# Performance work log

Hardware: AMD Instinct MI355X
Metric: run time of the kernel (lower is better)

The kernel has to match this reference:

```python
import jax, jax.numpy as jnp
import numpy as np

EMBED_DIM = 1024


def setup_inputs() -> dict:
    key = jax.random.key(0)
    ks = jax.random.split(key, 9)
    d = EMBED_DIM
    s = 1.0 / np.sqrt(d)
    x = jax.random.normal(ks[0], (4, 4096, d), dtype=jnp.float32)
    Wq = jax.random.normal(ks[1], (d, d), dtype=jnp.float32) * s
    bq = jax.random.normal(ks[2], (d,), dtype=jnp.float32) * 0.01
    Wk = jax.random.normal(ks[3], (d, d), dtype=jnp.float32) * s
    bk = jax.random.normal(ks[4], (d,), dtype=jnp.float32) * 0.01
    Wv = jax.random.normal(ks[5], (d, d), dtype=jnp.float32) * s
    bv = jax.random.normal(ks[6], (d,), dtype=jnp.float32) * 0.01
    Wo = jax.random.normal(ks[7], (d, d), dtype=jnp.float32) * s
    bo = jax.random.normal(ks[8], (d,), dtype=jnp.float32) * 0.01
    return {"x": x, "Wq": Wq, "bq": bq, "Wk": Wk, "bk": bk,
            "Wv": Wv, "bv": bv, "Wo": Wo, "bo": bo}


def reference(x, Wq, bq, Wk, bk, Wv, bv, Wo, bo):
    # x: [b, s, d]; single-head attention, scale = 1/sqrt(d)
    b, s, d = x.shape
    q = x @ Wq + bq
    k = x @ Wk + bk
    v = x @ Wv + bv
    scale = 1.0 / jnp.sqrt(jnp.asarray(d, x.dtype))
    scores = jnp.einsum('bqd,bkd->bqk', q, k) * scale  # [b, s, s]
    causal = jnp.tril(jnp.ones((s, s), dtype=bool))
    scores = jnp.where(causal, scores, jnp.asarray(-jnp.inf, scores.dtype))
    attn = jax.nn.softmax(scores, axis=-1)
    ctx = jnp.einsum('bqk,bkd->bqd', attn, v)
    return ctx @ Wo + bo
```

## Files before the change

kernel.cpp:

```cpp
#include <hip/hip_runtime.h>


typedef unsigned short u16;
typedef __attribute__((ext_vector_type(4))) unsigned short u16x4;
typedef __attribute__((ext_vector_type(8))) unsigned short u16x8;
typedef __attribute__((ext_vector_type(8))) __bf16 bf16x8;
typedef __attribute__((ext_vector_type(4))) float f32x4;

typedef const __attribute__((address_space(1))) void* as1cp;
typedef __attribute__((address_space(3))) void* as3p;

struct GemmPtrs {
  const u16* A[4];
  const u16* B[4];
  const float* bias[4];
  void* C[4];
};
struct TransPtrs {
  const void* in[4];
  u16* out[4];
};
struct SmPtrs {
  u16* P[4];
};

__device__ __forceinline__ u16 f2bf(float f) {
  union { float f; unsigned int i; } c; c.f = f;
  unsigned int r = c.i + 0x7fffu + ((c.i >> 16) & 1u);
  return (u16)(r >> 16);
}
__device__ __forceinline__ float bf2f(u16 u) {
  union { unsigned int i; float f; } c; c.i = ((unsigned int)u) << 16;
  return c.f;
}

__global__ __launch_bounds__(256) void cast_f32_bf16(const float* __restrict__ in,
                                                     u16* __restrict__ out, int n4) {
  int i = blockIdx.x * blockDim.x + threadIdx.x;
  if (i >= n4) return;
  float4 v = ((const float4*)in)[i];
  u16x4 u;
  u.x = f2bf(v.x); u.y = f2bf(v.y); u.z = f2bf(v.z); u.w = f2bf(v.w);
  ((u16x4*)out)[i] = u;
}

template <bool IN_F32>
__global__ __launch_bounds__(256) void transpose_to_bf16(TransPtrs tp, int R, int C) {
  __shared__ u16 t[32][34];
  int z = blockIdx.z;
  int tx = threadIdx.x, ty = threadIdx.y;
  int c0 = blockIdx.x * 32, r0 = blockIdx.y * 32;
#pragma unroll
  for (int dy = 0; dy < 4; ++dy) {
    int r = r0 + ty + dy * 8;
    int c = c0 + tx;
    u16 hv;
    if (IN_F32) hv = f2bf(((const float*)tp.in[z])[(size_t)r * C + c]);
    else        hv = ((const u16*)tp.in[z])[(size_t)r * C + c];
    t[ty + dy * 8][tx] = hv;
  }
  __syncthreads();
  u16* op = tp.out[z];
#pragma unroll
  for (int dy = 0; dy < 4; ++dy) {
    int a = ty + dy * 8;
    op[(size_t)(c0 + a) * R + r0 + tx] = t[tx][a];
  }
}

__global__ __launch_bounds__(256) void softmax_causal(SmPtrs sp) {
  int row = blockIdx.x;
  u16* P = sp.P[blockIdx.y];
  int tid = threadIdx.x;
  int lane = tid & 63, wv = tid >> 6;
  u16x8* prow = (u16x8*)(P + (size_t)row * 4096);
  int nch = (row >> 3) + 1;
  int fend = ((row >> 7) + 1) << 4;
  int c0 = tid, c1 = tid + 256;
  bool a0 = c0 < nch, a1 = c1 < nch;
  float vals[16];
  float lmax = -3.0e38f;
  if (a0) {
    u16x8 u = prow[c0];
#pragma unroll
    for (int e = 0; e < 8; ++e) {
      float f = (c0 * 8 + e <= row) ? bf2f(u[e]) : -3.0e38f;
      vals[e] = f; lmax = fmaxf(lmax, f);
    }
  } else {
#pragma unroll
    for (int e = 0; e < 8; ++e) vals[e] = -3.0e38f;
  }
  if (a1) {
    u16x8 u = prow[c1];
#pragma unroll
    for (int e = 0; e < 8; ++e) {
      float f = (c1 * 8 + e <= row) ? bf2f(u[e]) : -3.0e38f;
      vals[8 + e] = f; lmax = fmaxf(lmax, f);
    }
  } else {
#pragma unroll
    for (int e = 0; e < 8; ++e) vals[8 + e] = -3.0e38f;
  }
  __shared__ float red[8];
#pragma unroll
  for (int off = 32; off > 0; off >>= 1) lmax = fmaxf(lmax, __shfl_down(lmax, off, 64));
  if (lane == 0) red[wv] = lmax;
  __syncthreads();
  float m2 = fmaxf(fmaxf(red[0], red[1]), fmaxf(red[2], red[3]));
  float lsum = 0.f;
#pragma unroll
  for (int e = 0; e < 16; ++e) {
    float ev = __expf(vals[e] - m2);
    vals[e] = ev;
    lsum += ev;
  }
#pragma unroll
  for (int off = 32; off > 0; off >>= 1) lsum += __shfl_down(lsum, off, 64);
  if (lane == 0) red[4 + wv] = lsum;
  __syncthreads();
  float inv = 1.0f / (red[4] + red[5] + red[6] + red[7]);
  if (a0) {
    u16x8 u;
#pragma unroll
    for (int e = 0; e < 8; ++e) u[e] = f2bf(vals[e] * inv);
    prow[c0] = u;
  }
  if (a1) {
    u16x8 u;
#pragma unroll
    for (int e = 0; e < 8; ++e) u[e] = f2bf(vals[8 + e] * inv);
    prow[c1] = u;
  }
  u16x8 zz = (u16x8)(u16)0;
  for (int c = nch + tid; c < fend; c += 256) prow[c] = zz;
}

template <int MODE, bool OUT_BF16, bool HAS_BIAS, int MAXSLOT, int KDIM, int LDB>
__global__ __launch_bounds__(256) void gemm_persist(GemmPtrs p, int N, float cscale) {
  __shared__ __align__(16) u16 As[2][128 * 64];
  __shared__ __align__(16) u16 Bs[2][128 * 64];
  int b = blockIdx.x;
  int x = b & 7, q = b >> 3;
  int tid = threadIdx.x, lane = tid & 63, wv = tid >> 6;
  int wm = (wv >> 1) * 64, wn = (wv & 1) * 64;
  int lrow = lane & 15, lquad = lane >> 4;
  int srow = lane >> 3, scol = ((lane & 7) ^ srow) * 8;

  struct TP { const u16* A; const u16* B; int niter, tm, tn, z; };
  auto tileOf = [&](int s) {
    TP t;
    if (MODE == 0) {
      int c = x + 8 * (s * 8 + (q >> 3));
      t.z = c >> 7;
      t.tm = (c & 127) << 7; t.tn = (q & 7) << 7; t.niter = KDIM >> 6;
    } else if (MODE == 1) {
      int c = x + 8 * (s * 8 + (q >> 3));
      int tt = c * 8 + (q & 7);
      t.z = tt / 528; int L = tt - t.z * 528;
      int i = (int)((__fsqrt_rn(8.f * (float)L + 1.f) - 1.f) * 0.5f);
      while ((i + 1) * (i + 2) / 2 <= L) ++i;
      while (i * (i + 1) / 2 > L) --i;
      t.tm = i << 7; t.tn = (L - ((i * (i + 1)) >> 1)) << 7; t.niter = KDIM >> 6;
    } else if (MODE == 2) {
      int w = q & 15, h = w >> 3;
      int i = (s == 0) ? (h ? 15 - x : x) : (h ? 16 + x : 31 - x);
      t.z = q >> 4; t.tm = i << 7; t.tn = (w & 7) << 7; t.niter = (i + 1) * 2;
    } else {
      int c = x + 8 * (s * 8 + (q >> 3));
      t.z = 0; t.tm = c << 7; t.tn = (q & 7) << 7; t.niter = KDIM >> 6;
    }
    t.A = p.A[t.z] + (size_t)t.tm * KDIM;
    t.B = p.B[t.z] + (size_t)t.tn * LDB;
    return t;
  };
  int nslot = (MODE == 1) ? ((q >> 3) == 0 ? 5 : 4) : MAXSLOT;
  int total = (MODE == 2) ? 66 : nslot * (KDIM >> 6);

  int aoff = (wv * 32 + srow) * KDIM + scol;
  int boff = (wv * 32 + srow) * LDB + scol;

  TP st = tileOf(0);
  int stk = 0, sslot = 0;
  const u16* gA = st.A + aoff;
  const u16* gB = st.B + boff;

  auto stageTo = [&](int sb) {
#pragma unroll
    for (int tt = 0; tt < 4; ++tt) {
      __builtin_amdgcn_global_load_lds((as1cp)(gA + tt * 8 * KDIM),
                                       (as3p)&As[sb][(wv * 4 + tt) * 512], 16, 0, 0);
      __builtin_amdgcn_global_load_lds((as1cp)(gB + tt * 8 * LDB),
                                       (as3p)&Bs[sb][(wv * 4 + tt) * 512], 16, 0, 0);
    }
  };
  auto adv = [&]() {
    gA += 64; gB += 64;
    if (++stk == st.niter) {
      stk = 0;
      if (++sslot < nslot) {
        st = tileOf(sslot);
        gA = st.A + aoff;
        gB = st.B + boff;
      }
    }
  };

  f32x4 acc[4][4];
#pragma unroll
  for (int i = 0; i < 4; ++i)
#pragma unroll
    for (int j = 0; j < 4; ++j) acc[i][j] = (f32x4){0.f, 0.f, 0.f, 0.f};

  auto compute = [&](int cb) __attribute__((always_inline)) {
#pragma unroll
    for (int ks = 0; ks < 64; ks += 32) {
      bf16x8 af[4], bg[4];
#pragma unroll
      for (int mt = 0; mt < 4; ++mt) {
        int r = wm + mt * 16 + lrow;
        int jb = (ks >> 3) + lquad;
        af[mt] = *(const bf16x8*)&As[cb][r * 64 + ((jb ^ (r & 7)) << 3)];
      }
#pragma unroll
      for (int nt = 0; nt < 4; ++nt) {
        int r = wn + nt * 16 + lrow;
        int jb = (ks >> 3) + lquad;
        bg[nt] = *(const bf16x8*)&Bs[cb][r * 64 + ((jb ^ (r & 7)) << 3)];
      }
#pragma unroll
      for (int mt = 0; mt < 4; ++mt)
#pragma unroll
        for (int nt = 0; nt < 4; ++nt)
          acc[mt][nt] = __builtin_amdgcn_mfma_f32_16x16x32_bf16(af[mt], bg[nt], acc[mt][nt], 0, 0, 0);
    }
  };

  TP ct = st;
  int cit = 0, cslot = 0;
  auto epi = [&]() {
    if (++cit == ct.niter) {
      const float* bias = HAS_BIAS ? p.bias[ct.z] : nullptr;
#pragma unroll
      for (int mt = 0; mt < 4; ++mt) {
#pragma unroll
        for (int reg = 0; reg < 4; ++reg) {
          int r = ct.tm + wm + mt * 16 + lquad * 4 + reg;
#pragma unroll
          for (int nt = 0; nt < 4; ++nt) {
            int cidx = ct.tn + wn + nt * 16 + lrow;
            float vvv = acc[mt][nt][reg] * cscale;
            if (HAS_BIAS) vvv += bias[cidx];
            if (OUT_BF16) ((u16*)p.C[ct.z])[(size_t)r * N + cidx] = f2bf(vvv);
            else          ((float*)p.C[ct.z])[(size_t)r * N + cidx] = vvv;
          }
        }
      }
#pragma unroll
      for (int i = 0; i < 4; ++i)
#pragma unroll
        for (int j = 0; j < 4; ++j) acc[i][j] = (f32x4){0.f, 0.f, 0.f, 0.f};
      cit = 0;
      if (++cslot < nslot) ct = tileOf(cslot);
    }
  };

  stageTo(0);
  adv();
  for (int it = 0; it < total; it += 2) {
    if (it + 1 < total) {
      stageTo(1);
      adv();
      asm volatile("s_waitcnt vmcnt(8)" ::: "memory");
    } else {
      asm volatile("s_waitcnt vmcnt(0)" ::: "memory");
    }
    asm volatile("s_barrier" ::: "memory");
    compute(0);
    asm volatile("s_barrier" ::: "memory");
    epi();
    if (it + 2 < total) {
      stageTo(0);
      adv();
      asm volatile("s_waitcnt vmcnt(8)" ::: "memory");
    } else {
      asm volatile("s_waitcnt vmcnt(0)" ::: "memory");
    }
    asm volatile("s_barrier" ::: "memory");
    compute(1);
    asm volatile("s_barrier" ::: "memory");
    epi();
  }
}

extern "C" void kernel_launch(void* const* d_in, const int* in_sizes, int n_in,
                              void* d_out, int out_size, void* d_ws, size_t ws_size,
                              hipStream_t stream) {
  const float* x  = (const float*)d_in[0];
  const float* Wq = (const float*)d_in[1];
  const float* bq = (const float*)d_in[2];
  const float* Wk = (const float*)d_in[3];
  const float* bk = (const float*)d_in[4];
  const float* Wv = (const float*)d_in[5];
  const float* bv = (const float*)d_in[6];
  const float* Wo = (const float*)d_in[7];
  const float* bo = (const float*)d_in[8];

  const int S = 4096, D = 1024;
  const size_t XE = (size_t)4 * S * D;
  const size_t BSE = (size_t)S * D;

  char* ws = (char*)d_ws;
  u16* xb  = (u16*)(ws + 0);
  u16* q   = (u16*)(ws + 33554432);
  u16* k   = (u16*)(ws + 67108864);
  u16* v   = (u16*)(ws + 100663296);
  u16* ctx = (u16*)(ws + 134217728);
  u16* wqT = (u16*)(ws + 167772160);
  u16* wkT = wqT + 1048576;
  u16* wvT = wkT + 1048576;
  u16* woT = wvT + 1048576;
  u16* attn2 = (u16*)(ws + 176160768);
  u16* attn0 = (u16*)d_out;
  u16* attn1 = attn0 + (size_t)S * S;
  u16* attn3 = v;
  u16* vT = xb;
  u16* attn[4] = {attn0, attn1, attn2, attn3};

  cast_f32_bf16<<<(int)(XE / 4 / 256), 256, 0, stream>>>(x, xb, (int)(XE / 4));
  {
    TransPtrs tp = {{Wq, Wk, Wv, Wo}, {wqT, wkT, wvT, woT}};
    transpose_to_bf16<true><<<dim3(32, 32, 4), dim3(32, 8), 0, stream>>>(tp, D, D);
  }
  {
    GemmPtrs gp = {{xb, xb, xb, xb}, {wqT, wkT, wvT, wqT},
                   {bq, bk, bv, bq}, {q, k, v, q}};
    gemm_persist<0, true, true, 6, 1024, 1024><<<512, 256, 0, stream>>>(gp, D, 1.0f);
  }
  {
    TransPtrs tp = {{v, v + BSE, v + 2 * BSE, v + 3 * BSE},
                    {vT, vT + BSE, vT + 2 * BSE, vT + 3 * BSE}};
    transpose_to_bf16<false><<<dim3(D / 32, S / 32, 4), dim3(32, 8), 0, stream>>>(tp, S, D);
  }
  {
    GemmPtrs gp = {{q, q + BSE, q + 2 * BSE, q + 3 * BSE},
                   {k, k + BSE, k + 2 * BSE, k + 3 * BSE},
                   {nullptr, nullptr, nullptr, nullptr},
                   {attn[0], attn[1], attn[2], attn[3]}};
    gemm_persist<1, true, false, 5, 1024, 1024><<<512, 256, 0, stream>>>(gp, S, 0.03125f);
  }
  {
    SmPtrs sp = {{attn[0], attn[1], attn[2], attn[3]}};
    softmax_causal<<<dim3(S, 4), 256, 0, stream>>>(sp);
  }
  {
    GemmPtrs gp = {{attn[0], attn[1], attn[2], attn[3]},
                   {vT, vT + BSE, vT + 2 * BSE, vT + 3 * BSE},
                   {nullptr, nullptr, nullptr, nullptr},
                   {ctx, ctx + BSE, ctx + 2 * BSE, ctx + 3 * BSE}};
    gemm_persist<2, true, false, 2, 4096, 4096><<<512, 256, 0, stream>>>(gp, D, 1.0f);
  }
  {
    GemmPtrs gp = {{ctx, ctx, ctx, ctx}, {woT, woT, woT, woT},
                   {bo, bo, bo, bo}, {d_out, d_out, d_out, d_out}};
    gemm_persist<3, false, true, 2, 1024, 1024><<<512, 256, 0, stream>>>(gp, D, 1.0f);
  }
}
```

Before: 520.0 us.

## Add 256x256-tile persistent GEMM with 4-stage LDS pipeline for K=1024 GEMMs

Introduces a new persistent GEMM kernel that uses 256x256 output tiles, 512-thread blocks, a 4-slot direct-to-LDS pipeline and MFMA priority hints. It replaces the 128x128 kernel for the QKV projection, the causal QK^T scores (upper-triangle tile mapping) and the output projection. Larger tiles raise arithmetic intensity and cut global traffic. The cost is heavier register and LDS pressure and coarser load balance, with fewer tiles per GEMM.

```diff
diff --git a/kernel.cpp b/kernel.cpp
--- a/kernel.cpp
+++ b/kernel.cpp
@@ -134,6 +134,150 @@
   }
   u16x8 zz = (u16x8)(u16)0;
   for (int c = nch + tid; c < fend; c += 256) prow[c] = zz;
+}
+
+template <int MODE, bool OUT_BF16, bool HAS_BIAS>
+__global__ __launch_bounds__(512, 2) void gemm256(GemmPtrs p, int N, float cscale) {
+  __shared__ __align__(16) u16 As[4][8192];
+  __shared__ __align__(16) u16 Bs[4][8192];
+  const int b = blockIdx.x;
+  const int tid = threadIdx.x, lane = tid & 63, wv = tid >> 6;
+  const int wm = (wv >> 2) << 7, wn = (wv & 3) << 6;
+  const int lrow = lane & 15, lquad = lane >> 4;
+  const int xs = (lquad ^ ((lrow >> 1) & 3)) << 3;
+  const int aoff0 = (wm + lrow) * 32 + xs;
+  const int boff0 = (wn + lrow) * 32 + xs;
+  const int soff = (tid >> 2) * 1024 + (((tid & 3) ^ ((tid >> 3) & 3)) << 3);
+  const int nslot = (MODE == 1) ? (b < 32 ? 3 : 2) : (MODE == 0 ? 3 : 1);
+
+  struct TP { const u16* A; const u16* B; int tm, tn, z; };
+  auto tileOf = [&](int s) {
+    TP t;
+    if (MODE == 0) {
+      int g = s * 256 + b;
+      t.z = g >> 8; int i = g & 255;
+      t.tm = (i >> 2) << 8; t.tn = (i & 3) << 8;
+    } else if (MODE == 1) {
+      int g = s * 256 + b;
+      t.z = g / 136; int L = g - t.z * 136;
+      int i = (int)((__fsqrt_rn(8.f * (float)L + 1.f) - 1.f) * 0.5f);
+      while ((i + 1) * (i + 2) / 2 <= L) ++i;
+      while (i * (i + 1) / 2 > L) --i;
+      t.tm = i << 8; t.tn = (L - ((i * (i + 1)) >> 1)) << 8;
+    } else {
+      t.z = 0; t.tm = (b >> 2) << 8; t.tn = (b & 3) << 8;
+    }
+    t.A = p.A[t.z] + (size_t)t.tm * 1024;
+    t.B = p.B[t.z] + (size_t)t.tn * 1024;
+    return t;
+  };
+
+  auto stageA = [&](int slot, const u16* src) __attribute__((always_inline)) {
+    __builtin_amdgcn_global_load_lds((as1cp)src, (as3p)&As[slot][wv * 512], 16, 0, 0);
+    __builtin_amdgcn_global_load_lds((as1cp)(src + 131072),
+                                     (as3p)&As[slot][4096 + wv * 512], 16, 0, 0);
+  };
+  auto stageB = [&](int slot, const u16* src) __attribute__((always_inline)) {
+    __builtin_amdgcn_global_load_lds((as1cp)src, (as3p)&Bs[slot][wv * 512], 16, 0, 0);
+    __builtin_amdgcn_global_load_lds((as1cp)(src + 131072),
+                                     (as3p)&Bs[slot][4096 + wv * 512], 16, 0, 0);
+  };
+
+  f32x4 acc[8][4];
+
+  auto doBlock = [&](int tu, bool stg, const u16* sA, const u16* sB, int vm)
+      __attribute__((always_inline)) {
+    const int sT = (tu + 2) & 3;
+    bf16x8 af[4], bg[4];
+#pragma unroll
+    for (int m = 0; m < 4; ++m) af[m] = *(const bf16x8*)&As[tu][aoff0 + m * 512];
+#pragma unroll
+    for (int n = 0; n < 4; ++n) bg[n] = *(const bf16x8*)&Bs[tu][boff0 + n * 512];
+    if (stg) stageA(sT, sA);
+    asm volatile("s_barrier" ::: "memory");
+    __builtin_amdgcn_s_setprio(1);
+#pragma unroll
+    for (int m = 0; m < 4; ++m)
+#pragma unroll
+      for (int n = 0; n < 4; ++n)
+        acc[m][n] = __builtin_amdgcn_mfma_f32_16x16x32_bf16(af[m], bg[n], acc[m][n], 0, 0, 0);
+    __builtin_amdgcn_s_setprio(0);
+    asm volatile("s_barrier" ::: "memory");
+#pragma unroll
+    for (int m = 0; m < 4; ++m) af[m] = *(const bf16x8*)&As[tu][aoff0 + 2048 + m * 512];
+    if (stg) stageB(sT, sB);
+    asm volatile("s_barrier" ::: "memory");
+    __builtin_amdgcn_s_setprio(1);
+#pragma unroll
+    for (int m = 0; m < 4; ++m)
+#pragma unroll
+      for (int n = 0; n < 4; ++n)
+        acc[4 + m][n] = __builtin_amdgcn_mfma_f32_16x16x32_bf16(af[m], bg[n], acc[4 + m][n], 0, 0, 0);
+    __builtin_amdgcn_s_setprio(0);
+    if (vm == 4)      asm volatile("s_waitcnt vmcnt(4)" ::: "memory");
+    else if (vm == 0) asm volatile("s_waitcnt vmcnt(0)" ::: "memory");
+    asm volatile("s_barrier" ::: "memory");
+  };
+
+  TP ct = tileOf(0);
+  const u16* gA = ct.A + soff;
+  const u16* gB = ct.B + soff;
+  stageA(0, gA); stageB(0, gB);
+  stageA(1, gA + 32); stageB(1, gB + 32);
+  asm volatile("s_waitcnt vmcnt(4)" ::: "memory");
+  asm volatile("s_barrier" ::: "memory");
+
+  for (int s = 0;;) {
+#pragma unroll
+    for (int i = 0; i < 8; ++i)
+#pragma unroll
+      for (int j = 0; j < 4; ++j) acc[i][j] = (f32x4){0.f, 0.f, 0.f, 0.f};
+
+    for (int u = 0; u < 7; ++u) {
+#pragma unroll
+      for (int tu = 0; tu < 4; ++tu)
+        doBlock(tu, true, gA + (tu + 2) * 32, gB + (tu + 2) * 32, 4);
+      gA += 128; gB += 128;
+    }
+    doBlock(0, true, gA + 64, gB + 64, 4);
+    doBlock(1, true, gA + 96, gB + 96, 4);
+    doBlock(2, false, nullptr, nullptr, 0);
+    doBlock(3, false, nullptr, nullptr, -1);
+
+    bool more = (++s < nslot);
+    TP nt2;
+    if (more) {
+      nt2 = tileOf(s);
+      gA = nt2.A + soff; gB = nt2.B + soff;
+      stageA(0, gA); stageB(0, gB);
+    }
+    {
+      float bvv[4] = {0.f, 0.f, 0.f, 0.f};
+      if (HAS_BIAS) {
+        const float* bias = p.bias[ct.z];
+#pragma unroll
+        for (int n = 0; n < 4; ++n) bvv[n] = bias[ct.tn + wn + n * 16 + lrow];
+      }
+#pragma unroll
+      for (int m = 0; m < 8; ++m)
+#pragma unroll
+        for (int r = 0; r < 4; ++r) {
+          size_t row = (size_t)(ct.tm + wm + m * 16 + lquad * 4 + r);
+#pragma unroll
+          for (int n = 0; n < 4; ++n) {
+            int col = ct.tn + wn + n * 16 + lrow;
+            float vvv = acc[m][n][r] * cscale + bvv[n];
+            if (OUT_BF16) ((u16*)p.C[ct.z])[row * N + col] = f2bf(vvv);
+            else          ((float*)p.C[ct.z])[row * N + col] = vvv;
+          }
+        }
+    }
+    if (!more) return;
+    stageA(1, gA + 32); stageB(1, gB + 32);
+    asm volatile("s_waitcnt vmcnt(4)" ::: "memory");
+    asm volatile("s_barrier" ::: "memory");
+    ct = nt2;
+  }
 }
 
 template <int MODE, bool OUT_BF16, bool HAS_BIAS, int MAXSLOT, int KDIM, int LDB>
@@ -335,7 +479,7 @@
   {
     GemmPtrs gp = {{xb, xb, xb, xb}, {wqT, wkT, wvT, wqT},
                    {bq, bk, bv, bq}, {q, k, v, q}};
-    gemm_persist<0, true, true, 6, 1024, 1024><<<512, 256, 0, stream>>>(gp, D, 1.0f);
+    gemm256<0, true, true><<<256, 512, 0, stream>>>(gp, D, 1.0f);
   }
   {
     TransPtrs tp = {{v, v + BSE, v + 2 * BSE, v + 3 * BSE},
@@ -347,7 +491,7 @@
                    {k, k + BSE, k + 2 * BSE, k + 3 * BSE},
                    {nullptr, nullptr, nullptr, nullptr},
                    {attn[0], attn[1], attn[2], attn[3]}};
-    gemm_persist<1, true, false, 5, 1024, 1024><<<512, 256, 0, stream>>>(gp, S, 0.03125f);
+    gemm256<1, true, false><<<256, 512, 0, stream>>>(gp, S, 0.03125f);
   }
   {
     SmPtrs sp = {{attn[0], attn[1], attn[2], attn[3]}};
@@ -363,6 +507,6 @@
   {
     GemmPtrs gp = {{ctx, ctx, ctx, ctx}, {woT, woT, woT, woT},
                    {bo, bo, bo, bo}, {d_out, d_out, d_out, d_out}};
-    gemm_persist<3, false, true, 2, 1024, 1024><<<512, 256, 0, stream>>>(gp, D, 1.0f);
-  }
-}
+    gemm256<3, false, true><<<256, 512, 0, stream>>>(gp, D, 1.0f);
+  }
+}
```

Result: no change. 523.6 us (+0.7%).

## Replace persistent GEMM with 256x256-tile 512-thread kernel and dedicated PV kernel

Applied to the files above, without the earlier changes.

Replaces the 128x128, 256-thread persistent GEMM with a 256x256-tile, 8-wave kernel. It uses a 4-stage LDS ring with a K-step of 32, interleaved MFMA and LDS fragment loads, and s_setprio around the MFMA bursts. The causal P·V GEMM gets its own 128x256-tile kernel that pairs row blocks j and 31-j to balance the triangular work. The larger tiles raise arithmetic intensity and cut global traffic, and the deeper pipeline hides load latency. In exchange, register and LDS pressure go up, occupancy and the tile scheduling change, and the tile indexing is more intricate.

```diff
diff --git a/kernel.cpp b/kernel.cpp
--- a/kernel.cpp
+++ b/kernel.cpp
@@ -9,6 +9,8 @@
 
 typedef const __attribute__((address_space(1))) void* as1cp;
 typedef __attribute__((address_space(3))) void* as3p;
+
+template <int N> struct IC { static constexpr int v = N; };
 
 struct GemmPtrs {
   const u16* A[4];
@@ -136,161 +138,284 @@
   for (int c = nch + tid; c < fend; c += 256) prow[c] = zz;
 }
 
-template <int MODE, bool OUT_BF16, bool HAS_BIAS, int MAXSLOT, int KDIM, int LDB>
-__global__ __launch_bounds__(256) void gemm_persist(GemmPtrs p, int N, float cscale) {
-  __shared__ __align__(16) u16 As[2][128 * 64];
-  __shared__ __align__(16) u16 Bs[2][128 * 64];
-  int b = blockIdx.x;
-  int x = b & 7, q = b >> 3;
-  int tid = threadIdx.x, lane = tid & 63, wv = tid >> 6;
-  int wm = (wv >> 1) * 64, wn = (wv & 1) * 64;
-  int lrow = lane & 15, lquad = lane >> 4;
-  int srow = lane >> 3, scol = ((lane & 7) ^ srow) * 8;
-
-  struct TP { const u16* A; const u16* B; int niter, tm, tn, z; };
+template <int MODE, bool OUT_BF16, bool HAS_BIAS>
+__global__ __launch_bounds__(512, 2) void gemm256p(GemmPtrs p, int N, float cscale) {
+  __shared__ __align__(16) u16 As[4][8192];
+  __shared__ __align__(16) u16 Bs[4][8192];
+  const int b = blockIdx.x;
+  const int tid = threadIdx.x, lane = tid & 63, wv = tid >> 6;
+  const int wm = (wv >> 2) << 7, wn = (wv & 3) << 6;
+  const int lrow = lane & 15, lquad = lane >> 4;
+  const int xs = (lquad ^ ((lrow >> 1) & 3)) << 3;
+  const int aoff0 = (wm + lrow) * 32 + xs;
+  const int boff0 = (wn + lrow) * 32 + xs;
+  const int soff = (tid >> 2) * 1024 + (((tid & 3) ^ ((tid >> 3) & 3)) << 3);
+  const int x = b & 7, u = b >> 3;
+  const int nslot = (MODE == 1) ? (u < 4 ? 3 : 2) : (MODE == 0 ? 3 : 1);
+
+  struct TP { const u16* A; const u16* B; int tm, tn, z; };
   auto tileOf = [&](int s) {
     TP t;
     if (MODE == 0) {
-      int c = x + 8 * (s * 8 + (q >> 3));
-      t.z = c >> 7;
-      t.tm = (c & 127) << 7; t.tn = (q & 7) << 7; t.niter = KDIM >> 6;
+      int i = x * 32 + u;
+      t.z = s; t.tm = (i >> 2) << 8; t.tn = (i & 3) << 8;
     } else if (MODE == 1) {
-      int c = x + 8 * (s * 8 + (q >> 3));
-      int tt = c * 8 + (q & 7);
-      t.z = tt / 528; int L = tt - t.z * 528;
+      int g = x * 68 + s * 32 + u;
+      t.z = g / 136; int L = g - t.z * 136;
       int i = (int)((__fsqrt_rn(8.f * (float)L + 1.f) - 1.f) * 0.5f);
       while ((i + 1) * (i + 2) / 2 <= L) ++i;
       while (i * (i + 1) / 2 > L) --i;
-      t.tm = i << 7; t.tn = (L - ((i * (i + 1)) >> 1)) << 7; t.niter = KDIM >> 6;
-    } else if (MODE == 2) {
-      int w = q & 15, h = w >> 3;
-      int i = (s == 0) ? (h ? 15 - x : x) : (h ? 16 + x : 31 - x);
-      t.z = q >> 4; t.tm = i << 7; t.tn = (w & 7) << 7; t.niter = (i + 1) * 2;
+      t.tm = i << 8; t.tn = (L - ((i * (i + 1)) >> 1)) << 8;
     } else {
-      int c = x + 8 * (s * 8 + (q >> 3));
-      t.z = 0; t.tm = c << 7; t.tn = (q & 7) << 7; t.niter = KDIM >> 6;
-    }
-    t.A = p.A[t.z] + (size_t)t.tm * KDIM;
-    t.B = p.B[t.z] + (size_t)t.tn * LDB;
+      int i = x * 32 + u;
+      t.z = 0; t.tm = (i >> 2) << 8; t.tn = (i & 3) << 8;
+    }
+    t.A = p.A[t.z] + (size_t)t.tm * 1024;
+    t.B = p.B[t.z] + (size_t)t.tn * 1024;
     return t;
   };
-  int nslot = (MODE == 1) ? ((q >> 3) == 0 ? 5 : 4) : MAXSLOT;
-  int total = (MODE == 2) ? 66 : nslot * (KDIM >> 6);
-
-  int aoff = (wv * 32 + srow) * KDIM + scol;
-  int boff = (wv * 32 + srow) * LDB + scol;
-
-  TP st = tileOf(0);
-  int stk = 0, sslot = 0;
-  const u16* gA = st.A + aoff;
-  const u16* gB = st.B + boff;
-
-  auto stageTo = [&](int sb) {
-#pragma unroll
-    for (int tt = 0; tt < 4; ++tt) {
-      __builtin_amdgcn_global_load_lds((as1cp)(gA + tt * 8 * KDIM),
-                                       (as3p)&As[sb][(wv * 4 + tt) * 512], 16, 0, 0);
-      __builtin_amdgcn_global_load_lds((as1cp)(gB + tt * 8 * LDB),
-                                       (as3p)&Bs[sb][(wv * 4 + tt) * 512], 16, 0, 0);
-    }
-  };
+
+  const u16* gA; const u16* gB; int stk = 0, sslot = 0;
+  {
+    TP t0 = tileOf(0);
+    gA = t0.A + soff; gB = t0.B + soff;
+  }
   auto adv = [&]() {
-    gA += 64; gB += 64;
-    if (++stk == st.niter) {
-      stk = 0;
-      if (++sslot < nslot) {
-        st = tileOf(sslot);
-        gA = st.A + aoff;
-        gB = st.B + boff;
+    gA += 32; gB += 32;
+    ++stk;
+    if (stk == 32 && sslot < nslot) {
+      stk = 0; ++sslot;
+      if (sslot < nslot) {
+        TP t = tileOf(sslot);
+        gA = t.A + soff; gB = t.B + soff;
       }
     }
   };
 
-  f32x4 acc[4][4];
-#pragma unroll
-  for (int i = 0; i < 4; ++i)
+  f32x4 acc[8][4];
+#pragma unroll
+  for (int i = 0; i < 8; ++i)
 #pragma unroll
     for (int j = 0; j < 4; ++j) acc[i][j] = (f32x4){0.f, 0.f, 0.f, 0.f};
 
-  auto compute = [&](int cb) __attribute__((always_inline)) {
-#pragma unroll
-    for (int ks = 0; ks < 64; ks += 32) {
-      bf16x8 af[4], bg[4];
-#pragma unroll
-      for (int mt = 0; mt < 4; ++mt) {
-        int r = wm + mt * 16 + lrow;
-        int jb = (ks >> 3) + lquad;
-        af[mt] = *(const bf16x8*)&As[cb][r * 64 + ((jb ^ (r & 7)) << 3)];
-      }
-#pragma unroll
-      for (int nt = 0; nt < 4; ++nt) {
-        int r = wn + nt * 16 + lrow;
-        int jb = (ks >> 3) + lquad;
-        bg[nt] = *(const bf16x8*)&Bs[cb][r * 64 + ((jb ^ (r & 7)) << 3)];
-      }
-#pragma unroll
-      for (int mt = 0; mt < 4; ++mt)
-#pragma unroll
-        for (int nt = 0; nt < 4; ++nt)
-          acc[mt][nt] = __builtin_amdgcn_mfma_f32_16x16x32_bf16(af[mt], bg[nt], acc[mt][nt], 0, 0, 0);
-    }
-  };
-
-  TP ct = st;
-  int cit = 0, cslot = 0;
-  auto epi = [&]() {
-    if (++cit == ct.niter) {
-      const float* bias = HAS_BIAS ? p.bias[ct.z] : nullptr;
-#pragma unroll
-      for (int mt = 0; mt < 4; ++mt) {
-#pragma unroll
-        for (int reg = 0; reg < 4; ++reg) {
-          int r = ct.tm + wm + mt * 16 + lquad * 4 + reg;
-#pragma unroll
-          for (int nt = 0; nt < 4; ++nt) {
-            int cidx = ct.tn + wn + nt * 16 + lrow;
-            float vvv = acc[mt][nt][reg] * cscale;
-            if (HAS_BIAS) vvv += bias[cidx];
-            if (OUT_BF16) ((u16*)p.C[ct.z])[(size_t)r * N + cidx] = f2bf(vvv);
-            else          ((float*)p.C[ct.z])[(size_t)r * N + cidx] = vvv;
-          }
+  bf16x8 alo[4], ahi[4], bg0[4], bg1[4];
+
+#pragma unroll
+  for (int pt = 0; pt < 3; ++pt) {
+    __builtin_amdgcn_global_load_lds((as1cp)gA, (as3p)(As[pt] + wv * 512), 16, 0, 0);
+    __builtin_amdgcn_global_load_lds((as1cp)(gA + 131072), (as3p)(As[pt] + 4096 + wv * 512), 16, 0, 0);
+    __builtin_amdgcn_global_load_lds((as1cp)gB, (as3p)(Bs[pt] + wv * 512), 16, 0, 0);
+    __builtin_amdgcn_global_load_lds((as1cp)(gB + 131072), (as3p)(Bs[pt] + 4096 + wv * 512), 16, 0, 0);
+    adv();
+  }
+  asm volatile("s_waitcnt vmcnt(8)" ::: "memory");
+  asm volatile("s_barrier" ::: "memory");
+#pragma unroll
+  for (int m = 0; m < 4; ++m) alo[m] = *(const bf16x8*)&As[0][aoff0 + m * 512];
+#pragma unroll
+  for (int n = 0; n < 4; ++n) bg0[n] = *(const bf16x8*)&Bs[0][boff0 + n * 512];
+
+  auto kt = [&](auto CC, auto SS, auto VV, auto& BU, auto& BL)
+      __attribute__((always_inline)) {
+    constexpr int c = decltype(CC)::v;
+    constexpr int stg = decltype(SS)::v;
+    constexpr int vm = decltype(VV)::v;
+    __builtin_amdgcn_s_setprio(1);
+#pragma unroll
+    for (int m = 0; m < 4; ++m)
+#pragma unroll
+      for (int n = 0; n < 4; ++n)
+        acc[m][n] = __builtin_amdgcn_mfma_f32_16x16x32_bf16(alo[m], BU[n], acc[m][n], 0, 0, 0);
+    __builtin_amdgcn_s_setprio(0);
+#pragma unroll
+    for (int m = 0; m < 4; ++m)
+      ahi[m] = *(const bf16x8*)&As[c][aoff0 + 2048 + m * 512];
+    if constexpr (stg) {
+      __builtin_amdgcn_global_load_lds((as1cp)gA, (as3p)(As[(c + 3) & 3] + wv * 512), 16, 0, 0);
+      __builtin_amdgcn_global_load_lds((as1cp)(gA + 131072), (as3p)(As[(c + 3) & 3] + 4096 + wv * 512), 16, 0, 0);
+    }
+    if constexpr (vm == 6) asm volatile("s_waitcnt vmcnt(6)" ::: "memory");
+    else if constexpr (vm == 4) asm volatile("s_waitcnt vmcnt(4)" ::: "memory");
+    else if constexpr (vm == 0) asm volatile("s_waitcnt vmcnt(0)" ::: "memory");
+    asm volatile("s_barrier" ::: "memory");
+    __builtin_amdgcn_s_setprio(1);
+#pragma unroll
+    for (int m = 0; m < 4; ++m)
+#pragma unroll
+      for (int n = 0; n < 4; ++n)
+        acc[4 + m][n] = __builtin_amdgcn_mfma_f32_16x16x32_bf16(ahi[m], BU[n], acc[4 + m][n], 0, 0, 0);
+    __builtin_amdgcn_s_setprio(0);
+#pragma unroll
+    for (int m = 0; m < 4; ++m)
+      alo[m] = *(const bf16x8*)&As[(c + 1) & 3][aoff0 + m * 512];
+#pragma unroll
+    for (int n = 0; n < 4; ++n)
+      BL[n] = *(const bf16x8*)&Bs[(c + 1) & 3][boff0 + n * 512];
+    if constexpr (stg) {
+      __builtin_amdgcn_global_load_lds((as1cp)gB, (as3p)(Bs[(c + 3) & 3] + wv * 512), 16, 0, 0);
+      __builtin_amdgcn_global_load_lds((as1cp)(gB + 131072), (as3p)(Bs[(c + 3) & 3] + 4096 + wv * 512), 16, 0, 0);
+      adv();
+    }
+    asm volatile("s_barrier" ::: "memory");
+  };
+
+  auto epi = [&](int cs2) {
+    TP t = tileOf(cs2);
+    float bvv[4] = {0.f, 0.f, 0.f, 0.f};
+    if constexpr (HAS_BIAS) {
+#pragma unroll
+      for (int n = 0; n < 4; ++n) bvv[n] = p.bias[t.z][t.tn + wn + n * 16 + lrow];
+    }
+#pragma unroll
+    for (int m = 0; m < 8; ++m)
+#pragma unroll
+      for (int r = 0; r < 4; ++r) {
+        size_t row = (size_t)(t.tm + wm + m * 16 + lquad * 4 + r);
+#pragma unroll
+        for (int n = 0; n < 4; ++n) {
+          int col = t.tn + wn + n * 16 + lrow;
+          float vvv = acc[m][n][r] * cscale + bvv[n];
+          if (OUT_BF16) ((u16*)p.C[t.z])[row * N + col] = f2bf(vvv);
+          else          ((float*)p.C[t.z])[row * N + col] = vvv;
         }
       }
 #pragma unroll
-      for (int i = 0; i < 4; ++i)
-#pragma unroll
-        for (int j = 0; j < 4; ++j) acc[i][j] = (f32x4){0.f, 0.f, 0.f, 0.f};
-      cit = 0;
-      if (++cslot < nslot) ct = tileOf(cslot);
-    }
-  };
-
-  stageTo(0);
-  adv();
-  for (int it = 0; it < total; it += 2) {
-    if (it + 1 < total) {
-      stageTo(1);
-      adv();
-      asm volatile("s_waitcnt vmcnt(8)" ::: "memory");
-    } else {
-      asm volatile("s_waitcnt vmcnt(0)" ::: "memory");
-    }
+    for (int m2 = 0; m2 < 8; ++m2)
+#pragma unroll
+      for (int n2 = 0; n2 < 4; ++n2) acc[m2][n2] = (f32x4){0.f, 0.f, 0.f, 0.f};
+  };
+
+  const int total = nslot * 32;
+  int cs = 0;
+  for (int G = 0; G + 4 < total; G += 4) {
+    kt(IC<0>{}, IC<1>{}, IC<6>{}, bg0, bg1);
+    kt(IC<1>{}, IC<1>{}, IC<6>{}, bg1, bg0);
+    kt(IC<2>{}, IC<1>{}, IC<6>{}, bg0, bg1);
+    kt(IC<3>{}, IC<1>{}, IC<6>{}, bg1, bg0);
+    if (((G + 4) & 31) == 0) { epi(cs); ++cs; }
+  }
+  kt(IC<0>{}, IC<1>{}, IC<6>{}, bg0, bg1);
+  kt(IC<1>{}, IC<0>{}, IC<4>{}, bg1, bg0);
+  kt(IC<2>{}, IC<0>{}, IC<0>{}, bg0, bg1);
+  kt(IC<3>{}, IC<0>{}, IC<-1>{}, bg1, bg0);
+  epi(nslot - 1);
+}
+
+__global__ __launch_bounds__(512, 2) void gemm_pv(GemmPtrs p) {
+  __shared__ __align__(16) u16 As[4][4096];
+  __shared__ __align__(16) u16 Bs[4][8192];
+  const int b = blockIdx.x;
+  const int tid = threadIdx.x, lane = tid & 63, wv = tid >> 6;
+  const int wm = (wv >> 2) << 6, wn = (wv & 3) << 6;
+  const int lrow = lane & 15, lquad = lane >> 4;
+  const int xs = (lquad ^ ((lrow >> 1) & 3)) << 3;
+  const int aoff0 = (wm + lrow) * 32 + xs;
+  const int boff0 = (wn + lrow) * 32 + xs;
+  const int soff = (tid >> 2) * 4096 + (((tid & 3) ^ ((tid >> 3) & 3)) << 3);
+  const int x = b & 7, u = b >> 3;
+  const int P = x * 32 + u;
+  const int z = P >> 6, j = (P >> 2) & 15, n4 = P & 3;
+  const int i1 = j, i2 = 31 - j;
+  const int tn = n4 << 8;
+  const int T1 = (i1 + 1) * 4;
+  const int niter1 = (i2 + 1) * 4;
+  const u16* Abase = p.A[z];
+  const u16* Bbase = p.B[z] + (size_t)tn * 4096;
+
+  const u16* gA = Abase + (size_t)(i1 << 7) * 4096 + soff;
+  const u16* gB = Bbase + soff;
+  int stk = 0, sslot = 0;
+  auto adv = [&]() {
+    gA += 32; gB += 32;
+    ++stk;
+    if (sslot == 0 && stk == T1) {
+      stk = 0; sslot = 1;
+      gA = Abase + (size_t)(i2 << 7) * 4096 + soff;
+      gB = Bbase + soff;
+    } else if (sslot == 1 && stk == niter1) {
+      stk = 0; sslot = 2;
+    }
+  };
+
+  f32x4 acc[4][4];
+#pragma unroll
+  for (int i = 0; i < 4; ++i)
+#pragma unroll
+    for (int jj = 0; jj < 4; ++jj) acc[i][jj] = (f32x4){0.f, 0.f, 0.f, 0.f};
+
+  bf16x8 a0[4], a1[4], b0[4], b1[4];
+
+  auto stage = [&](int slot) __attribute__((always_inline)) {
+    __builtin_amdgcn_global_load_lds((as1cp)gA, (as3p)(As[slot] + wv * 512), 16, 0, 0);
+    __builtin_amdgcn_global_load_lds((as1cp)gB, (as3p)(Bs[slot] + wv * 512), 16, 0, 0);
+    __builtin_amdgcn_global_load_lds((as1cp)(gB + 524288), (as3p)(Bs[slot] + 4096 + wv * 512), 16, 0, 0);
+    adv();
+  };
+
+  stage(0); stage(1); stage(2);
+  asm volatile("s_waitcnt vmcnt(3)" ::: "memory");
+  asm volatile("s_barrier" ::: "memory");
+#pragma unroll
+  for (int m = 0; m < 4; ++m) a0[m] = *(const bf16x8*)&As[0][aoff0 + m * 512];
+#pragma unroll
+  for (int n = 0; n < 4; ++n) b0[n] = *(const bf16x8*)&Bs[0][boff0 + n * 512];
+
+  auto kt = [&](auto CC, auto SS, auto VV, auto& AU, auto& BU, auto& AL, auto& BL)
+      __attribute__((always_inline)) {
+    constexpr int c = decltype(CC)::v;
+    constexpr int stg = decltype(SS)::v;
+    constexpr int vm = decltype(VV)::v;
+    __builtin_amdgcn_s_setprio(1);
+#pragma unroll
+    for (int m = 0; m < 4; ++m)
+#pragma unroll
+      for (int n = 0; n < 4; ++n)
+        acc[m][n] = __builtin_amdgcn_mfma_f32_16x16x32_bf16(AU[m], BU[n], acc[m][n], 0, 0, 0);
+    __builtin_amdgcn_s_setprio(0);
+#pragma unroll
+    for (int m = 0; m < 4; ++m)
+      AL[m] = *(const bf16x8*)&As[(c + 1) & 3][aoff0 + m * 512];
+#pragma unroll
+    for (int n = 0; n < 4; ++n)
+      BL[n] = *(const bf16x8*)&Bs[(c + 1) & 3][boff0 + n * 512];
+    if constexpr (stg) stage((c + 3) & 3);
+    if constexpr (vm == 3) asm volatile("s_waitcnt vmcnt(3)" ::: "memory");
+    else if constexpr (vm == 0) asm volatile("s_waitcnt vmcnt(0)" ::: "memory");
     asm volatile("s_barrier" ::: "memory");
-    compute(0);
-    asm volatile("s_barrier" ::: "memory");
-    epi();
-    if (it + 2 < total) {
-      stageTo(0);
-      adv();
-      asm volatile("s_waitcnt vmcnt(8)" ::: "memory");
-    } else {
-      asm volatile("s_waitcnt vmcnt(0)" ::: "memory");
-    }
-    asm volatile("s_barrier" ::: "memory");
-    compute(1);
-    asm volatile("s_barrier" ::: "memory");
-    epi();
-  }
+  };
+
+  auto epi = [&](int s) {
+    int tm = (s ? i2 : i1) << 7;
+#pragma unroll
+    for (int m = 0; m < 4; ++m)
+#pragma unroll
+      for (int r = 0; r < 4; ++r) {
+        size_t row = (size_t)(tm + wm + m * 16 + lquad * 4 + r);
+#pragma unroll
+        for (int n = 0; n < 4; ++n) {
+          int col = tn + wn + n * 16 + lrow;
+          ((u16*)p.C[z])[row * 1024 + col] = f2bf(acc[m][n][r]);
+        }
+      }
+#pragma unroll
+    for (int m2 = 0; m2 < 4; ++m2)
+#pragma unroll
+      for (int n2 = 0; n2 < 4; ++n2) acc[m2][n2] = (f32x4){0.f, 0.f, 0.f, 0.f};
+  };
+
+  const int total = 132;
+  for (int G = 0; G + 4 < total; G += 4) {
+    kt(IC<0>{}, IC<1>{}, IC<3>{}, a0, b0, a1, b1);
+    kt(IC<1>{}, IC<1>{}, IC<3>{}, a1, b1, a0, b0);
+    kt(IC<2>{}, IC<1>{}, IC<3>{}, a0, b0, a1, b1);
+    kt(IC<3>{}, IC<1>{}, IC<3>{}, a1, b1, a0, b0);
+    if (G + 4 == T1) epi(0);
+  }
+  kt(IC<0>{}, IC<1>{}, IC<3>{}, a0, b0, a1, b1);
+  kt(IC<1>{}, IC<0>{}, IC<3>{}, a1, b1, a0, b0);
+  kt(IC<2>{}, IC<0>{}, IC<0>{}, a0, b0, a1, b1);
+  kt(IC<3>{}, IC<0>{}, IC<-1>{}, a1, b1, a0, b0);
+  epi(1);
 }
 
 extern "C" void kernel_launch(void* const* d_in, const int* in_sizes, int n_in,
@@ -335,7 +460,7 @@
   {
     GemmPtrs gp = {{xb, xb, xb, xb}, {wqT, wkT, wvT, wqT},
                    {bq, bk, bv, bq}, {q, k, v, q}};
-    gemm_persist<0, true, true, 6, 1024, 1024><<<512, 256, 0, stream>>>(gp, D, 1.0f);
+    gemm256p<0, true, true><<<256, 512, 0, stream>>>(gp, D, 1.0f);
   }
   {
     TransPtrs tp = {{v, v + BSE, v + 2 * BSE, v + 3 * BSE},
@@ -347,7 +472,7 @@
                    {k, k + BSE, k + 2 * BSE, k + 3 * BSE},
                    {nullptr, nullptr, nullptr, nullptr},
                    {attn[0], attn[1], attn[2], attn[3]}};
-    gemm_persist<1, true, false, 5, 1024, 1024><<<512, 256, 0, stream>>>(gp, S, 0.03125f);
+    gemm256p<1, true, false><<<256, 512, 0, stream>>>(gp, S, 0.03125f);
   }
   {
     SmPtrs sp = {{attn[0], attn[1], attn[2], attn[3]}};
@@ -358,11 +483,11 @@
                    {vT, vT + BSE, vT + 2 * BSE, vT + 3 * BSE},
                    {nullptr, nullptr, nullptr, nullptr},
                    {ctx, ctx + BSE, ctx + 2 * BSE, ctx + 3 * BSE}};
-    gemm_persist<2, true, false, 2, 4096, 4096><<<512, 256, 0, stream>>>(gp, D, 1.0f);
+    gemm_pv<<<256, 512, 0, stream>>>(gp);
   }
   {
     GemmPtrs gp = {{ctx, ctx, ctx, ctx}, {woT, woT, woT, woT},
                    {bo, bo, bo, bo}, {d_out, d_out, d_out, d_out}};
-    gemm_persist<3, false, true, 2, 1024, 1024><<<512, 256, 0, stream>>>(gp, D, 1.0f);
-  }
-}
+    gemm256p<3, false, true><<<256, 512, 0, stream>>>(gp, D, 1.0f);
+  }
+}
```

Result: no change. 522.4 us (+0.5%).
